# Optimization experiments

Hardware: AMD Instinct MI355X
Metric: run time of the kernel (lower is better)

## Reference

```python
import jax, jax.numpy as jnp
import numpy as np

B, N = 4, 512
H, NH, L = 64, 4, 3
HD = H // NH          # 16
NODE_F, EDGE_F = 18, 7
H4 = H // 4           # 16
FF = 4 * H            # 256


def _ln(x, g, b, eps=1e-5):
    m = jnp.mean(x, axis=-1, keepdims=True)
    v = jnp.mean((x - m) ** 2, axis=-1, keepdims=True)
    return (x - m) * jax.lax.rsqrt(v + eps) * g + b


def _leaky(x):
    return jnp.where(x >= 0, x, 0.2 * x)


def _spd(edge_mask):
    # Vectorized Floyd-Warshall, mirrors GraphTransformer._compute_spd_matrix
    n = edge_mask.shape[1]
    spd = jnp.where(edge_mask, 1.0, float(n)).astype(jnp.float32)
    i = jnp.arange(n)
    spd = spd.at[:, i, i].set(0.0)
    def body(k, s):
        col = jax.lax.dynamic_slice_in_dim(s, k, 1, axis=2)  # [B,N,1]
        row = jax.lax.dynamic_slice_in_dim(s, k, 1, axis=1)  # [B,1,N]
        return jnp.minimum(s, col + row)
    return jax.lax.fori_loop(0, n, body, spd)


def setup_inputs() -> dict:
    key = jax.random.key(0)
    ks = iter(jax.random.split(key, 64))
    def nrm(shape, s):
        return jax.random.normal(next(ks), shape, jnp.float32) * s
    inp = {}
    inp["node_features"] = jax.random.normal(next(ks), (B, N, NODE_F), jnp.float32)
    inp["edge_features"] = jax.random.normal(next(ks), (B, N, N, EDGE_F), jnp.float32)
    nm = jax.random.uniform(next(ks), (B, N)) < 0.9
    inp["node_mask"] = nm.at[:, 0].set(True)
    inp["edge_mask"] = jax.random.uniform(next(ks), (B, N, N)) < 0.05
    s_h = 1.0 / np.sqrt(H)
    inp["node_proj_w"] = nrm((NODE_F, H), 0.2)
    inp["node_proj_b"] = jnp.zeros((H,), jnp.float32)
    inp["edge_proj_w"] = nrm((EDGE_F, H), 0.2)
    inp["edge_proj_b"] = jnp.zeros((H,), jnp.float32)
    inp["wq"] = nrm((L, H, H), s_h)
    inp["wk"] = nrm((L, H, H), s_h)
    inp["wv"] = nrm((L, H, H), s_h)
    inp["eb1_w"] = nrm((L, H, H4), s_h)
    inp["eb1_b"] = jnp.zeros((L, H4), jnp.float32)
    inp["eb_ln_g"] = jnp.ones((L, H4), jnp.float32)
    inp["eb_ln_b"] = jnp.zeros((L, H4), jnp.float32)
    inp["eb2_w"] = nrm((L, H4, NH), 0.2)
    inp["eb2_b"] = jnp.zeros((L, NH), jnp.float32)
    inp["spd1_w"] = nrm((L, 1, H4), 0.5)
    inp["spd1_b"] = jnp.zeros((L, H4), jnp.float32)
    inp["spd2_w"] = nrm((L, H4, NH), 0.2)
    inp["spd2_b"] = jnp.zeros((L, NH), jnp.float32)
    inp["wo_w"] = nrm((L, H, H), s_h)
    inp["wo_b"] = jnp.zeros((L, H), jnp.float32)
    inp["ln1_g"] = jnp.ones((L, H), jnp.float32)
    inp["ln1_b"] = jnp.zeros((L, H), jnp.float32)
    inp["ln2_g"] = jnp.ones((L, H), jnp.float32)
    inp["ln2_b"] = jnp.zeros((L, H), jnp.float32)
    inp["ffn1_w"] = nrm((L, H, FF), s_h)
    inp["ffn1_b"] = jnp.zeros((L, FF), jnp.float32)
    inp["ffn2_w"] = nrm((L, FF, H), 1.0 / np.sqrt(FF))
    inp["ffn2_b"] = jnp.zeros((L, H), jnp.float32)
    inp["score1_w"] = nrm((2 * H, H), 1.0 / np.sqrt(2 * H))
    inp["score1_b"] = jnp.zeros((H,), jnp.float32)
    inp["score_ln_g"] = jnp.ones((H,), jnp.float32)
    inp["score_ln_b"] = jnp.zeros((H,), jnp.float32)
    inp["score2_w"] = nrm((H, 1), 0.1)
    inp["score2_b"] = jnp.zeros((1,), jnp.float32)
    return inp


def reference(node_features, edge_features, node_mask, edge_mask,
              node_proj_w, node_proj_b, edge_proj_w, edge_proj_b,
              wq, wk, wv,
              eb1_w, eb1_b, eb_ln_g, eb_ln_b, eb2_w, eb2_b,
              spd1_w, spd1_b, spd2_w, spd2_b,
              wo_w, wo_b, ln1_g, ln1_b, ln2_g, ln2_b,
              ffn1_w, ffn1_b, ffn2_w, ffn2_b,
              score1_w, score1_b, score_ln_g, score_ln_b, score2_w, score2_b):
    NEG = -1000000000.0
    h = node_features @ node_proj_w + node_proj_b            # [B,N,H]
    e = edge_features @ edge_proj_w + edge_proj_b            # [B,N,N,H]
    spd = _spd(edge_mask)
    spd_n = (jnp.clip(spd, 0.0, 10.0) / 10.0)[..., None]      # [B,N,N,1]
    scale = 1.0 / np.sqrt(HD)
    for l in range(L):
        Q = (h @ wq[l]).reshape(B, N, NH, HD)
        K = (h @ wk[l]).reshape(B, N, NH, HD)
        V = (h @ wv[l]).reshape(B, N, NH, HD)
        scores = jnp.einsum('bihd,bjhd->bhij', Q, K) * scale  # [B,NH,N,N]
        x = _leaky(_ln(e @ eb1_w[l] + eb1_b[l], eb_ln_g[l], eb_ln_b[l]))
        edge_bias = jnp.transpose(x @ eb2_w[l] + eb2_b[l], (0, 3, 1, 2))
        sb = _leaky(spd_n @ spd1_w[l] + spd1_b[l]) @ spd2_w[l] + spd2_b[l]
        spd_bias = jnp.transpose(sb, (0, 3, 1, 2))
        bias = jnp.where(edge_mask[:, None, :, :], edge_bias, spd_bias)
        scores = jnp.where(node_mask[:, None, None, :], scores + bias, NEG)
        attn = jax.nn.softmax(scores, axis=-1)
        out = jnp.einsum('bhij,bjhd->bihd', attn, V).reshape(B, N, H)
        out = out @ wo_w[l] + wo_b[l]
        h = _ln(h + out, ln1_g[l], ln1_b[l])
        ff = jax.nn.gelu(h @ ffn1_w[l] + ffn1_b[l], approximate=False) @ ffn2_w[l] + ffn2_b[l]
        h = _ln(h + ff, ln2_g[l], ln2_b[l])
    h_ego = jnp.broadcast_to(h[:, :1, :], (B, N - 1, H))
    hc = jnp.concatenate([h_ego, h[:, 1:, :]], axis=-1)       # [B,N-1,2H]
    x = _leaky(_ln(hc @ score1_w + score1_b, score_ln_g, score_ln_b))
    logits = (x @ score2_w + score2_b)[..., 0]                # [B,N-1]
    cand_mask = node_mask[:, 1:]
    no_cand = ~jnp.any(cand_mask, axis=-1)
    cand_mask = cand_mask.at[:, 0].set(cand_mask[:, 0] | no_cand)
    logits = jnp.where(cand_mask, logits, NEG)
    probs = jax.nn.softmax(logits, axis=-1)
    return probs, h
```

## Files before the change

### kernel.cpp

```cpp
#include <hip/hip_runtime.h>
#include <math.h>

typedef unsigned long long u64;
typedef unsigned int u32;

__device__ __forceinline__ float wsum(float x) {
#pragma unroll
    for (int o = 1; o < 64; o <<= 1) x += __shfl_xor(x, o);
    return x;
}
__device__ __forceinline__ float wmaxr(float x) {
#pragma unroll
    for (int o = 1; o < 64; o <<= 1) x = fmaxf(x, __shfl_xor(x, o));
    return x;
}

__global__ __launch_bounds__(256) void kA(
    const int* __restrict__ em, const float* __restrict__ nf,
    const float* __restrict__ npw, const float* __restrict__ npb,
    u64* __restrict__ adj, u32* __restrict__ elist, u32* __restrict__ rowCnt,
    float* __restrict__ hbuf)
{
    int t = threadIdx.x, wv = t >> 6, lane = t & 63;
    int g = blockIdx.x * 4 + wv;
    const int* emr = em + (size_t)g * 512;
    u32 run = 0;
#pragma unroll
    for (int s = 0; s < 8; ++s) {
        int j = s * 64 + lane;
        int v = emr[j];
        u64 bal = __ballot(v != 0);
        if (v != 0) {
            u32 slot = run + (u32)__popcll(bal & ((1ULL << lane) - 1ULL));
            if (slot < 96u) elist[g * 96 + slot] = (u32)j;
        }
        if (lane == 0) adj[(size_t)g * 8 + s] = bal;
        run += (u32)__popcll(bal);
    }
    if (lane == 0) rowCnt[g] = run < 96u ? run : 96u;
    float acc = npb[lane];
    const float* r = nf + (size_t)g * 18;
#pragma unroll
    for (int c = 0; c < 18; ++c) acc += r[c] * npw[c * 64 + lane];
    hbuf[(size_t)g * 64 + lane] = acc;
}

__global__ __launch_bounds__(256) void kB(
    const u64* __restrict__ adj, const float* __restrict__ ef,
    const u32* __restrict__ elist, const u32* __restrict__ rowCnt,
    const float* __restrict__ hbuf,
    const float* __restrict__ epw, const float* __restrict__ epb,
    const float* __restrict__ eb1w, const float* __restrict__ eb1b,
    const float* __restrict__ eblng, const float* __restrict__ eblnb,
    const float* __restrict__ eb2w, const float* __restrict__ eb2b,
    const float* __restrict__ wq, const float* __restrict__ wk, const float* __restrict__ wvw,
    unsigned char* __restrict__ spd, float* __restrict__ vals,
    float* __restrict__ Qb, float* __restrict__ KT, float* __restrict__ VT)
{
    __shared__ u64 adjL[4096];
    __shared__ u64 bfsS[4][24];
    __shared__ float MS[684];
    __shared__ u32 pool[384];
    __shared__ u32 offs[5];
    __shared__ u32 cA[4];
    __shared__ int votes[4];
    int t = threadIdx.x, wv = t >> 6, lane = t & 63;
    int g = blockIdx.x * 4 + wv;
    int b = g >> 9, srow = g & 511;
    {
        const float4* s = (const float4*)(adj + (size_t)b * 4096);
        float4* d = (float4*)adjL;
#pragma unroll
        for (int u = 0; u < 8; ++u) d[t + u * 256] = s[t + u * 256];
    }
    for (int u = t; u < 384; u += 256) {
        int l = u >> 7, r = u & 127, f = r >> 4, c = r & 15;
        const float* W1 = eb1w + l * 1024 + c;
        float s;
        if (f < 7) {
            s = 0.f;
            const float* ew = epw + f * 64;
            for (int k = 0; k < 64; ++k) s += ew[k] * W1[k * 16];
        } else {
            s = eb1b[l * 16 + c];
            for (int k = 0; k < 64; ++k) s += epb[k] * W1[k * 16];
        }
        MS[u] = s;
    }
    if (t < 192) MS[384 + t] = eb2w[t];
    if (t < 48) { MS[576 + t] = eblng[t]; MS[624 + t] = eblnb[t]; }
    if (t < 12) MS[672 + t] = eb2b[t];
    u64* vis = &bfsS[wv][0]; u64* fro = vis + 8; u64* nxt = vis + 16;
    if (lane < 8) {
        u64 iv = (lane == (srow >> 6)) ? (1ULL << (srow & 63)) : 0ULL;
        vis[lane] = iv; fro[lane] = iv; nxt[lane] = 0ULL;
    }
    __syncthreads();
    u64 myDist = 0x0A0A0A0A0A0A0A0AULL;
    if (lane == (srow >> 3)) myDist &= ~(0xFFULL << ((srow & 7) * 8));
    for (int d = 1; d <= 9; ++d) {
        int c = lane >> 3, w = lane & 7;
        u64 f = fro[c];
        u64 acc = 0ULL;
        while (f) {
            int k = (c << 6) + __builtin_ctzll(f);
            f &= f - 1;
            acc |= adjL[k * 8 + w];
        }
        if (acc) atomicOr(&nxt[w], acc);
        __syncthreads();
        u64 nw = 0ULL;
        if (lane < 8) {
            nw = nxt[lane] & ~vis[lane];
            vis[lane] |= nw; fro[lane] = nw; nxt[lane] = 0ULL;
        }
        u64 bal = __ballot(nw != 0ULL);
        if (lane == 0) votes[wv] = (bal != 0ULL) ? 1 : 0;
        __syncthreads();
        u64 fw = fro[lane >> 3];
        u32 bits = (u32)(fw >> ((lane & 7) * 8)) & 0xFFu;
        if (bits) {
            u64 bm = 0ULL;
#pragma unroll
            for (int kk = 0; kk < 8; ++kk) if (bits & (1u << kk)) bm |= 0xFFULL << (8 * kk);
            myDist = (myDist & ~bm) | ((0x0101010101010101ULL * (u64)(u32)d) & bm);
        }
        if (!(votes[0] | votes[1] | votes[2] | votes[3])) break;
    }
    ((u64*)spd)[(size_t)g * 64 + lane] = myDist;
    {
        float hv = hbuf[(size_t)g * 64 + lane];
        float aq = 0.f, ak = 0.f, av = 0.f;
        for (int k = 0; k < 64; ++k) {
            float hk = __shfl(hv, k);
            aq += hk * wq[k * 64 + lane];
            ak += hk * wk[k * 64 + lane];
            av += hk * wvw[k * 64 + lane];
        }
        Qb[(size_t)g * 64 + lane] = aq;
        KT[((size_t)(b * 64 + lane)) * 512 + srow] = ak;
        VT[((size_t)(b * 64 + lane)) * 512 + srow] = av;
    }
    u32 cnt = rowCnt[g];
    if (lane == 0) cA[wv] = cnt;
    __syncthreads();
    if (t == 0) {
        u32 a = 0;
        for (int i = 0; i < 4; ++i) { offs[i] = a; a += cA[i]; }
        offs[4] = a;
    }
    __syncthreads();
    u32 base = offs[wv];
    if (lane < (int)cnt)
        pool[base + lane] = ((u32)wv << 16) | ((u32)lane << 9) | elist[g * 96 + lane];
    if (lane + 64 < (int)cnt)
        pool[base + lane + 64] = ((u32)wv << 16) | ((u32)(lane + 64) << 9) | elist[g * 96 + lane + 64];
    __syncthreads();
    u32 tot = offs[4];
    for (u32 e = t; e < tot; e += 256) {
        u32 p = pool[e];
        int rl = (int)(p >> 16);
        u32 s = (p >> 9) & 127u;
        u32 j = p & 511u;
        int ge = blockIdx.x * 4 + rl;
        const float* e7 = ef + ((size_t)ge * 512 + j) * 7;
        float ff[7];
#pragma unroll
        for (int f = 0; f < 7; ++f) ff[f] = e7[f];
#pragma unroll 1
        for (int l = 0; l < 3; ++l) {
            float tt[16];
#pragma unroll
            for (int c = 0; c < 16; ++c) tt[c] = MS[(l * 8 + 7) * 16 + c];
#pragma unroll
            for (int f = 0; f < 7; ++f) {
                float fv = ff[f];
#pragma unroll
                for (int c = 0; c < 16; ++c) tt[c] += fv * MS[(l * 8 + f) * 16 + c];
            }
            float m = 0.f;
#pragma unroll
            for (int c = 0; c < 16; ++c) m += tt[c];
            m *= 0.0625f;
            float var = 0.f;
#pragma unroll
            for (int c = 0; c < 16; ++c) { float d = tt[c] - m; var += d * d; }
            var *= 0.0625f;
            float inv = rsqrtf(var + 1e-5f);
#pragma unroll
            for (int c = 0; c < 16; ++c) {
                float x = (tt[c] - m) * inv * MS[576 + l * 16 + c] + MS[624 + l * 16 + c];
                tt[c] = x >= 0.f ? x : 0.2f * x;
            }
#pragma unroll
            for (int hh = 0; hh < 4; ++hh) {
                float a = MS[672 + l * 4 + hh];
#pragma unroll
                for (int c = 0; c < 16; ++c) a += tt[c] * MS[384 + (l * 16 + c) * 4 + hh];
                vals[(u32)(l * 4 + hh) * 196608u + (u32)ge * 96u + s] = a;
            }
        }
    }
}

__global__ __launch_bounds__(256) void kAttn(
    const float* __restrict__ Qb, const float* __restrict__ KTin, const float* __restrict__ VTin,
    const unsigned char* __restrict__ spd, const u32* __restrict__ elist,
    const u32* __restrict__ rowCnt, const float* __restrict__ vals,
    const float* __restrict__ s1w, const float* __restrict__ s1b,
    const float* __restrict__ s2w, const float* __restrict__ s2b,
    const int* __restrict__ nm, int l, float* __restrict__ attO)
{
    __shared__ float kt[8192];
    __shared__ float bv[2048];
    int t = threadIdx.x, wv = t >> 6, lane = t & 63;
    int blk = blockIdx.x;
    int bh = blk >> 7, tile = blk & 127;
    int b = bh >> 2, hh = bh & 3;
    int rbase = tile * 4;
    int g = b * 512 + rbase + wv;
    {
        const float4* s = (const float4*)(KTin + ((size_t)(b * 64 + hh * 16)) * 512);
        float4* d = (float4*)kt;
#pragma unroll
        for (int u = 0; u < 8; ++u) d[t + u * 256] = s[t + u * 256];
    }
    float tval;
    {
        int li = lane < 11 ? lane : 10;
        float x = (float)li * 0.1f;
        float a = s2b[l * 4 + hh];
#pragma unroll
        for (int c = 0; c < 16; ++c) {
            float v = x * s1w[l * 16 + c] + s1b[l * 16 + c];
            v = v >= 0.f ? v : 0.2f * v;
            a += v * s2w[(l * 16 + c) * 4 + hh];
        }
        tval = a;
    }
    {
        const u32* sp = (const u32*)(spd + ((size_t)(b * 512 + rbase)) * 512);
#pragma unroll
        for (int p = 0; p < 2; ++p) {
            int i32 = t + p * 256;
            u32 w4 = sp[i32];
            float4 bb;
            bb.x = __shfl(tval, (int)(w4 & 255u));
            bb.y = __shfl(tval, (int)((w4 >> 8) & 255u));
            bb.z = __shfl(tval, (int)((w4 >> 16) & 255u));
            bb.w = __shfl(tval, (int)(w4 >> 24));
            ((float4*)bv)[i32] = bb;
        }
    }
    __syncthreads();
    u32 cnt = rowCnt[g];
    u32 vp = (u32)(l * 4 + hh) * 196608u;
    if (lane < (int)cnt) {
        u32 j = elist[g * 96 + lane];
        bv[wv * 512 + j] = vals[vp + (u32)g * 96u + lane];
    }
    if (lane + 64 < (int)cnt) {
        u32 j = elist[g * 96 + lane + 64];
        bv[wv * 512 + j] = vals[vp + (u32)g * 96u + lane + 64];
    }
    float madd[8];
#pragma unroll
    for (int c = 0; c < 8; ++c) madd[c] = (nm[b * 512 + c * 64 + lane] != 0) ? 0.f : -1e9f;
    float qrow = Qb[(size_t)g * 64 + lane];
    float q[16];
#pragma unroll
    for (int d = 0; d < 16; ++d) q[d] = __shfl(qrow, hh * 16 + d);
    float sc[8];
    float mx = -3e38f;
#pragma unroll
    for (int c = 0; c < 8; ++c) {
        int j = c * 64 + lane;
        float s = 0.f;
#pragma unroll
        for (int d = 0; d < 16; ++d) s += q[d] * kt[d * 512 + j];
        s = s * 0.25f + bv[wv * 512 + j] + madd[c];
        sc[c] = s;
        mx = fmaxf(mx, s);
    }
    mx = wmaxr(mx);
    float sm = 0.f;
#pragma unroll
    for (int c = 0; c < 8; ++c) { sc[c] = __expf(sc[c] - mx); sm += sc[c]; }
    float sminv = 1.0f / wsum(sm);
#pragma unroll
    for (int c = 0; c < 8; ++c) sc[c] *= sminv;
    __syncthreads();
    {
        const float4* s = (const float4*)(VTin + ((size_t)(b * 64 + hh * 16)) * 512);
        float4* d = (float4*)kt;
#pragma unroll
        for (int u = 0; u < 8; ++u) d[t + u * 256] = s[t + u * 256];
    }
    __syncthreads();
    float acc[16];
#pragma unroll
    for (int d = 0; d < 16; ++d) acc[d] = 0.f;
#pragma unroll
    for (int c = 0; c < 8; ++c) {
        int j = c * 64 + lane;
#pragma unroll
        for (int d = 0; d < 16; ++d) acc[d] += sc[c] * kt[d * 512 + j];
    }
#pragma unroll
    for (int d = 0; d < 16; ++d) {
        acc[d] += __shfl_xor(acc[d], 16);
        acc[d] += __shfl_xor(acc[d], 32);
    }
    float* scr = bv + wv * 272;
    if (lane < 16) {
#pragma unroll
        for (int d = 0; d < 16; ++d) scr[lane * 17 + d] = acc[d];
    }
    if (lane < 16) {
        float o = 0.f;
#pragma unroll
        for (int m = 0; m < 16; ++m) o += scr[m * 17 + lane];
        attO[(size_t)g * 64 + hh * 16 + lane] = o;
    }
}

__global__ __launch_bounds__(256) void kLF(
    const float* __restrict__ attO,
    const float* __restrict__ wow, const float* __restrict__ wob,
    const float* __restrict__ ln1g, const float* __restrict__ ln1b,
    const float* __restrict__ f1w, const float* __restrict__ f1b,
    const float* __restrict__ f2w, const float* __restrict__ f2b,
    const float* __restrict__ ln2g, const float* __restrict__ ln2b,
    const float* __restrict__ wqn, const float* __restrict__ wkn, const float* __restrict__ wvn,
    const float* __restrict__ sc1w, const float* __restrict__ sc1b,
    float* __restrict__ hbuf, float* __restrict__ QbOut,
    float* __restrict__ KTout, float* __restrict__ VTout,
    float* __restrict__ egoAcc, int l, float* __restrict__ out)
{
    int t = threadIdx.x, wv = t >> 6, lane = t & 63;
    int g = blockIdx.x * 4 + wv;
    int b = g >> 9, srow = g & 511;
    float hv = hbuf[(size_t)g * 64 + lane];
    float att = attO[(size_t)g * 64 + lane];
    float h1;
    {
        float a = wob[l * 64 + lane];
        const float* Wo = wow + l * 4096;
        for (int k = 0; k < 64; ++k) a += __shfl(att, k) * Wo[k * 64 + lane];
        float xx = a + hv;
        float mn = wsum(xx) * 0.015625f;
        float d = xx - mn;
        float var = wsum(d * d) * 0.015625f;
        h1 = d * rsqrtf(var + 1e-5f) * ln1g[l * 64 + lane] + ln1b[l * 64 + lane];
    }
    float hn;
    {
        const float* W1 = f1w + l * 16384;
        const float* W2 = f2w + l * 16384;
        float a1[4];
#pragma unroll
        for (int m = 0; m < 4; ++m) a1[m] = f1b[l * 256 + m * 64 + lane];
        for (int k = 0; k < 64; ++k) {
            float hk = __shfl(h1, k);
#pragma unroll
            for (int m = 0; m < 4; ++m) a1[m] += hk * W1[k * 256 + m * 64 + lane];
        }
        float ffv[4];
#pragma unroll
        for (int m = 0; m < 4; ++m) {
            float u = a1[m];
            ffv[m] = 0.5f * u * (1.0f + erff(u * 0.70710678118654752f));
        }
        float a2 = 0.f;
#pragma unroll 1
        for (int m = 0; m < 4; ++m) {
            for (int ll = 0; ll < 64; ++ll) {
                a2 += __shfl(ffv[m], ll) * W2[(m * 64 + ll) * 64 + lane];
            }
        }
        float xx = a2 + f2b[l * 64 + lane] + h1;
        float mn = wsum(xx) * 0.015625f;
        float d = xx - mn;
        float var = wsum(d * d) * 0.015625f;
        hn = d * rsqrtf(var + 1e-5f) * ln2g[l * 64 + lane] + ln2b[l * 64 + lane];
    }
    hbuf[(size_t)g * 64 + lane] = hn;
    if (l == 2) {
        out[2044 + (size_t)g * 64 + lane] = hn;
        if (srow == 0) {
            float ea = sc1b[lane];
            for (int k = 0; k < 64; ++k) ea += __shfl(hn, k) * sc1w[k * 64 + lane];
            egoAcc[b * 64 + lane] = ea;
        }
    } else {
        float aq = 0.f, ak = 0.f, av = 0.f;
        for (int k = 0; k < 64; ++k) {
            float hk = __shfl(hn, k);
            aq += hk * wqn[k * 64 + lane];
            ak += hk * wkn[k * 64 + lane];
            av += hk * wvn[k * 64 + lane];
        }
        QbOut[(size_t)g * 64 + lane] = aq;
        KTout[((size_t)(b * 64 + lane)) * 512 + srow] = ak;
        VTout[((size_t)(b * 64 + lane)) * 512 + srow] = av;
    }
}

__global__ __launch_bounds__(256) void kS(
    const float* __restrict__ hbuf, const float* __restrict__ egoAcc,
    const float* __restrict__ s1w,
    const float* __restrict__ lng, const float* __restrict__ lnb,
    const float* __restrict__ s2w, const float* __restrict__ s2b,
    float* __restrict__ logits)
{
    int t = threadIdx.x, wv = t >> 6, lane = t & 63;
    int wid = blockIdx.x * 4 + wv;
    if (wid >= 2044) return;
    int bb = wid / 511; int jj = wid % 511; int j = jj + 1;
    float cand = hbuf[((size_t)(bb * 512 + j)) * 64 + lane];
    float acc = egoAcc[bb * 64 + lane];
    for (int k = 0; k < 64; ++k) acc += __shfl(cand, k) * s1w[(64 + k) * 64 + lane];
    float mn = wsum(acc) * 0.015625f;
    float d = acc - mn;
    float var = wsum(d * d) * 0.015625f;
    float x = d * rsqrtf(var + 1e-5f) * lng[lane] + lnb[lane];
    x = x >= 0.f ? x : 0.2f * x;
    float p = wsum(x * s2w[lane]);
    if (lane == 0) logits[wid] = p + s2b[0];
}

__global__ __launch_bounds__(512) void kP(
    const float* __restrict__ logits, const int* __restrict__ nmask, float* __restrict__ out)
{
    __shared__ float red[512];
    __shared__ int anyf;
    int b = blockIdx.x; int t = threadIdx.x;
    bool cand = false;
    if (t < 511) cand = nmask[b * 512 + 1 + t] != 0;
    if (t == 0) anyf = 0;
    __syncthreads();
    if (cand) atomicOr(&anyf, 1);
    __syncthreads();
    if (t == 0 && anyf == 0) cand = true;
    float val = -3e38f;
    if (t < 511) val = cand ? logits[b * 511 + t] : -1e9f;
    red[t] = val; __syncthreads();
    for (int s = 256; s > 0; s >>= 1) { if (t < s) red[t] = fmaxf(red[t], red[t + s]); __syncthreads(); }
    float m = red[0]; __syncthreads();
    float p = (t < 511) ? __expf(val - m) : 0.f;
    red[t] = p; __syncthreads();
    for (int s = 256; s > 0; s >>= 1) { if (t < s) red[t] += red[t + s]; __syncthreads(); }
    float inv = 1.0f / red[0];
    if (t < 511) out[b * 511 + t] = p * inv;
}

extern "C" void kernel_launch(void* const* d_in, const int* in_sizes, int n_in,
                              void* d_out, int out_size, void* d_ws, size_t ws_size,
                              hipStream_t stream) {
    const float* nf    = (const float*)d_in[0];
    const float* ef    = (const float*)d_in[1];
    const int*   nm    = (const int*)d_in[2];
    const int*   em    = (const int*)d_in[3];
    const float* npw   = (const float*)d_in[4];
    const float* npb   = (const float*)d_in[5];
    const float* epw   = (const float*)d_in[6];
    const float* epb   = (const float*)d_in[7];
    const float* wq    = (const float*)d_in[8];
    const float* wk    = (const float*)d_in[9];
    const float* wv    = (const float*)d_in[10];
    const float* eb1w  = (const float*)d_in[11];
    const float* eb1b  = (const float*)d_in[12];
    const float* eblng = (const float*)d_in[13];
    const float* eblnb = (const float*)d_in[14];
    const float* eb2w  = (const float*)d_in[15];
    const float* eb2b  = (const float*)d_in[16];
    const float* s1wv  = (const float*)d_in[17];
    const float* s1bv  = (const float*)d_in[18];
    const float* s2wv  = (const float*)d_in[19];
    const float* s2bv  = (const float*)d_in[20];
    const float* wow   = (const float*)d_in[21];
    const float* wob   = (const float*)d_in[22];
    const float* ln1g  = (const float*)d_in[23];
    const float* ln1b  = (const float*)d_in[24];
    const float* ln2g  = (const float*)d_in[25];
    const float* ln2b  = (const float*)d_in[26];
    const float* f1w   = (const float*)d_in[27];
    const float* f1b   = (const float*)d_in[28];
    const float* f2w   = (const float*)d_in[29];
    const float* f2b   = (const float*)d_in[30];
    const float* sc1w  = (const float*)d_in[31];
    const float* sc1b  = (const float*)d_in[32];
    const float* sclng = (const float*)d_in[33];
    const float* sclnb = (const float*)d_in[34];
    const float* sc2w  = (const float*)d_in[35];
    const float* sc2b  = (const float*)d_in[36];

    char* W = (char*)d_ws;
    u64*   adj    = (u64*)(W + 0);
    unsigned char* spd = (unsigned char*)(W + 131072);
    u32*   elist  = (u32*)(W + 1179648);
    u32*   rowCnt = (u32*)(W + 1966080);
    float* vals   = (float*)(W + 1974272);
    float* hbuf   = (float*)(W + 11411456);
    float* Qb     = (float*)(W + 11935744);
    float* KT0    = (float*)(W + 12460032);
    float* VT0    = (float*)(W + 12984320);
    float* KT1    = (float*)(W + 13508608);
    float* VT1    = (float*)(W + 14032896);
    float* logits = (float*)(W + 14557184);
    float* egoAcc = (float*)(W + 14565376);
    float* attO   = (float*)(W + 14566400);

    float* out = (float*)d_out;

    kA<<<512, 256, 0, stream>>>(em, nf, npw, npb, adj, elist, rowCnt, hbuf);
    kB<<<512, 256, 0, stream>>>(adj, ef, elist, rowCnt, hbuf, epw, epb,
                                eb1w, eb1b, eblng, eblnb, eb2w, eb2b,
                                wq, wk, wv, spd, vals, Qb, KT0, VT0);

    kAttn<<<2048, 256, 0, stream>>>(Qb, KT0, VT0, spd, elist, rowCnt, vals,
                                    s1wv, s1bv, s2wv, s2bv, nm, 0, attO);
    kLF<<<512, 256, 0, stream>>>(attO, wow, wob, ln1g, ln1b, f1w, f1b, f2w, f2b,
                                 ln2g, ln2b, wq + 4096, wk + 4096, wv + 4096,
                                 sc1w, sc1b, hbuf, Qb, KT1, VT1, egoAcc, 0, out);

    kAttn<<<2048, 256, 0, stream>>>(Qb, KT1, VT1, spd, elist, rowCnt, vals,
                                    s1wv, s1bv, s2wv, s2bv, nm, 1, attO);
    kLF<<<512, 256, 0, stream>>>(attO, wow, wob, ln1g, ln1b, f1w, f1b, f2w, f2b,
                                 ln2g, ln2b, wq + 8192, wk + 8192, wv + 8192,
                                 sc1w, sc1b, hbuf, Qb, KT0, VT0, egoAcc, 1, out);

    kAttn<<<2048, 256, 0, stream>>>(Qb, KT0, VT0, spd, elist, rowCnt, vals,
                                    s1wv, s1bv, s2wv, s2bv, nm, 2, attO);
    kLF<<<512, 256, 0, stream>>>(attO, wow, wob, ln1g, ln1b, f1w, f1b, f2w, f2b,
                                 ln2g, ln2b, wq, wk, wv,
                                 sc1w, sc1b, hbuf, Qb, KT1, VT1, egoAcc, 2, out);

    kS<<<511, 256, 0, stream>>>(hbuf, egoAcc, s1wv ? sc1w : sc1w, sclng, sclnb, sc2w, sc2b, logits);
    kP<<<4, 512, 0, stream>>>(logits, nm, out);
}
```

Baseline: 315.8 us.

## Fuse per-layer attention into FFN kernel and merge scoring with softmax

Each layer's attention is folded into the layer/FFN kernel. Every block now loops serially over the four heads for its own four rows and keeps the attention output in shared memory, so the attO global round trip and one launch per layer go away. The candidate-scoring and final softmax kernels are merged into a single 4-block, 1024-thread kernel, with logits held in shared memory. In exchange, the attention grid shrinks from 2048 blocks to 512 and head processing is serialized, and the scoring stage runs on only four blocks. Both changes reduce parallelism.

```diff
diff --git a/kernel.cpp b/kernel.cpp
--- a/kernel.cpp
+++ b/kernel.cpp
@@ -203,129 +203,13 @@
     }
 }
 
-__global__ __launch_bounds__(256) void kAttn(
+__global__ __launch_bounds__(256, 2) void kL(
     const float* __restrict__ Qb, const float* __restrict__ KTin, const float* __restrict__ VTin,
     const unsigned char* __restrict__ spd, const u32* __restrict__ elist,
     const u32* __restrict__ rowCnt, const float* __restrict__ vals,
     const float* __restrict__ s1w, const float* __restrict__ s1b,
     const float* __restrict__ s2w, const float* __restrict__ s2b,
-    const int* __restrict__ nm, int l, float* __restrict__ attO)
-{
-    __shared__ float kt[8192];
-    __shared__ float bv[2048];
-    int t = threadIdx.x, wv = t >> 6, lane = t & 63;
-    int blk = blockIdx.x;
-    int bh = blk >> 7, tile = blk & 127;
-    int b = bh >> 2, hh = bh & 3;
-    int rbase = tile * 4;
-    int g = b * 512 + rbase + wv;
-    {
-        const float4* s = (const float4*)(KTin + ((size_t)(b * 64 + hh * 16)) * 512);
-        float4* d = (float4*)kt;
-#pragma unroll
-        for (int u = 0; u < 8; ++u) d[t + u * 256] = s[t + u * 256];
-    }
-    float tval;
-    {
-        int li = lane < 11 ? lane : 10;
-        float x = (float)li * 0.1f;
-        float a = s2b[l * 4 + hh];
-#pragma unroll
-        for (int c = 0; c < 16; ++c) {
-            float v = x * s1w[l * 16 + c] + s1b[l * 16 + c];
-            v = v >= 0.f ? v : 0.2f * v;
-            a += v * s2w[(l * 16 + c) * 4 + hh];
-        }
-        tval = a;
-    }
-    {
-        const u32* sp = (const u32*)(spd + ((size_t)(b * 512 + rbase)) * 512);
-#pragma unroll
-        for (int p = 0; p < 2; ++p) {
-            int i32 = t + p * 256;
-            u32 w4 = sp[i32];
-            float4 bb;
-            bb.x = __shfl(tval, (int)(w4 & 255u));
-            bb.y = __shfl(tval, (int)((w4 >> 8) & 255u));
-            bb.z = __shfl(tval, (int)((w4 >> 16) & 255u));
-            bb.w = __shfl(tval, (int)(w4 >> 24));
-            ((float4*)bv)[i32] = bb;
-        }
-    }
-    __syncthreads();
-    u32 cnt = rowCnt[g];
-    u32 vp = (u32)(l * 4 + hh) * 196608u;
-    if (lane < (int)cnt) {
-        u32 j = elist[g * 96 + lane];
-        bv[wv * 512 + j] = vals[vp + (u32)g * 96u + lane];
-    }
-    if (lane + 64 < (int)cnt) {
-        u32 j = elist[g * 96 + lane + 64];
-        bv[wv * 512 + j] = vals[vp + (u32)g * 96u + lane + 64];
-    }
-    float madd[8];
-#pragma unroll
-    for (int c = 0; c < 8; ++c) madd[c] = (nm[b * 512 + c * 64 + lane] != 0) ? 0.f : -1e9f;
-    float qrow = Qb[(size_t)g * 64 + lane];
-    float q[16];
-#pragma unroll
-    for (int d = 0; d < 16; ++d) q[d] = __shfl(qrow, hh * 16 + d);
-    float sc[8];
-    float mx = -3e38f;
-#pragma unroll
-    for (int c = 0; c < 8; ++c) {
-        int j = c * 64 + lane;
-        float s = 0.f;
-#pragma unroll
-        for (int d = 0; d < 16; ++d) s += q[d] * kt[d * 512 + j];
-        s = s * 0.25f + bv[wv * 512 + j] + madd[c];
-        sc[c] = s;
-        mx = fmaxf(mx, s);
-    }
-    mx = wmaxr(mx);
-    float sm = 0.f;
-#pragma unroll
-    for (int c = 0; c < 8; ++c) { sc[c] = __expf(sc[c] - mx); sm += sc[c]; }
-    float sminv = 1.0f / wsum(sm);
-#pragma unroll
-    for (int c = 0; c < 8; ++c) sc[c] *= sminv;
-    __syncthreads();
-    {
-        const float4* s = (const float4*)(VTin + ((size_t)(b * 64 + hh * 16)) * 512);
-        float4* d = (float4*)kt;
-#pragma unroll
-        for (int u = 0; u < 8; ++u) d[t + u * 256] = s[t + u * 256];
-    }
-    __syncthreads();
-    float acc[16];
-#pragma unroll
-    for (int d = 0; d < 16; ++d) acc[d] = 0.f;
-#pragma unroll
-    for (int c = 0; c < 8; ++c) {
-        int j = c * 64 + lane;
-#pragma unroll
-        for (int d = 0; d < 16; ++d) acc[d] += sc[c] * kt[d * 512 + j];
-    }
-#pragma unroll
-    for (int d = 0; d < 16; ++d) {
-        acc[d] += __shfl_xor(acc[d], 16);
-        acc[d] += __shfl_xor(acc[d], 32);
-    }
-    float* scr = bv + wv * 272;
-    if (lane < 16) {
-#pragma unroll
-        for (int d = 0; d < 16; ++d) scr[lane * 17 + d] = acc[d];
-    }
-    if (lane < 16) {
-        float o = 0.f;
-#pragma unroll
-        for (int m = 0; m < 16; ++m) o += scr[m * 17 + lane];
-        attO[(size_t)g * 64 + hh * 16 + lane] = o;
-    }
-}
-
-__global__ __launch_bounds__(256) void kLF(
-    const float* __restrict__ attO,
+    const int* __restrict__ nm,
     const float* __restrict__ wow, const float* __restrict__ wob,
     const float* __restrict__ ln1g, const float* __restrict__ ln1b,
     const float* __restrict__ f1w, const float* __restrict__ f1b,
@@ -337,16 +221,116 @@
     float* __restrict__ KTout, float* __restrict__ VTout,
     float* __restrict__ egoAcc, int l, float* __restrict__ out)
 {
+    __shared__ float kt[8192];
+    __shared__ float bv[2048];
+    __shared__ float ATTO[256];
     int t = threadIdx.x, wv = t >> 6, lane = t & 63;
-    int g = blockIdx.x * 4 + wv;
+    int blk = blockIdx.x;
+    int g = blk * 4 + wv;
     int b = g >> 9, srow = g & 511;
     float hv = hbuf[(size_t)g * 64 + lane];
-    float att = attO[(size_t)g * 64 + lane];
+    float qrow = Qb[(size_t)g * 64 + lane];
+    const unsigned char* sprow = spd + (size_t)g * 512;
+    unsigned char sb[8];
+#pragma unroll
+    for (int c = 0; c < 8; ++c) sb[c] = sprow[c * 64 + lane];
+    float madd[8];
+#pragma unroll
+    for (int c = 0; c < 8; ++c) madd[c] = (nm[b * 512 + c * 64 + lane] != 0) ? 0.f : -1e9f;
+    u32 cnt = rowCnt[g];
+    u32 ej0 = 0, ej1 = 0;
+    if (lane < (int)cnt) ej0 = elist[g * 96 + lane] & 511u;
+    if (lane + 64 < (int)cnt) ej1 = elist[g * 96 + lane + 64] & 511u;
+
+#pragma unroll 1
+    for (int hh = 0; hh < 4; ++hh) {
+        __syncthreads();
+        {
+            const float4* s = (const float4*)(KTin + ((size_t)(b * 64 + hh * 16)) * 512);
+            float4* d = (float4*)kt;
+#pragma unroll
+            for (int u = 0; u < 8; ++u) d[t + u * 256] = s[t + u * 256];
+        }
+        float tval;
+        {
+            int li = lane < 11 ? lane : 10;
+            float x = (float)li * 0.1f;
+            float a = s2b[l * 4 + hh];
+#pragma unroll
+            for (int c = 0; c < 16; ++c) {
+                float v = x * s1w[l * 16 + c] + s1b[l * 16 + c];
+                v = v >= 0.f ? v : 0.2f * v;
+                a += v * s2w[(l * 16 + c) * 4 + hh];
+            }
+            tval = a;
+        }
+#pragma unroll
+        for (int c = 0; c < 8; ++c) bv[wv * 512 + c * 64 + lane] = __shfl(tval, (int)sb[c]);
+        u32 vp = (u32)(l * 4 + hh) * 196608u;
+        if (lane < (int)cnt) bv[wv * 512 + ej0] = vals[vp + (u32)g * 96u + lane];
+        if (lane + 64 < (int)cnt) bv[wv * 512 + ej1] = vals[vp + (u32)g * 96u + lane + 64];
+        __syncthreads();
+        float q[16];
+#pragma unroll
+        for (int d = 0; d < 16; ++d) q[d] = __shfl(qrow, hh * 16 + d);
+        float sc[8];
+        float mx = -3e38f;
+#pragma unroll
+        for (int c = 0; c < 8; ++c) {
+            int j = c * 64 + lane;
+            float s = 0.f;
+#pragma unroll
+            for (int d = 0; d < 16; ++d) s += q[d] * kt[d * 512 + j];
+            s = s * 0.25f + bv[wv * 512 + j] + madd[c];
+            sc[c] = s;
+            mx = fmaxf(mx, s);
+        }
+        mx = wmaxr(mx);
+        float sm = 0.f;
+#pragma unroll
+        for (int c = 0; c < 8; ++c) { sc[c] = __expf(sc[c] - mx); sm += sc[c]; }
+        float sminv = 1.0f / wsum(sm);
+#pragma unroll
+        for (int c = 0; c < 8; ++c) sc[c] *= sminv;
+        __syncthreads();
+        {
+            const float4* s = (const float4*)(VTin + ((size_t)(b * 64 + hh * 16)) * 512);
+            float4* d = (float4*)kt;
+#pragma unroll
+            for (int u = 0; u < 8; ++u) d[t + u * 256] = s[t + u * 256];
+        }
+        __syncthreads();
+        float acc[16];
+#pragma unroll
+        for (int d = 0; d < 16; ++d) acc[d] = 0.f;
+#pragma unroll
+        for (int c = 0; c < 8; ++c) {
+            int j = c * 64 + lane;
+#pragma unroll
+            for (int d = 0; d < 16; ++d) acc[d] += sc[c] * kt[d * 512 + j];
+        }
+#pragma unroll
+        for (int d = 0; d < 16; ++d) {
+            acc[d] += __shfl_xor(acc[d], 16);
+            acc[d] += __shfl_xor(acc[d], 32);
+        }
+        float* scr = bv + wv * 272;
+        if (lane < 16) {
+#pragma unroll
+            for (int d = 0; d < 16; ++d) scr[lane * 17 + d] = acc[d];
+        }
+        if (lane < 16) {
+            float o = 0.f;
+#pragma unroll
+            for (int m = 0; m < 16; ++m) o += scr[m * 17 + lane];
+            ATTO[wv * 64 + hh * 16 + lane] = o;
+        }
+    }
     float h1;
     {
         float a = wob[l * 64 + lane];
         const float* Wo = wow + l * 4096;
-        for (int k = 0; k < 64; ++k) a += __shfl(att, k) * Wo[k * 64 + lane];
+        for (int k = 0; k < 64; ++k) a += ATTO[wv * 64 + k] * Wo[k * 64 + lane];
         float xx = a + hv;
         float mn = wsum(xx) * 0.015625f;
         float d = xx - mn;
@@ -406,50 +390,60 @@
     }
 }
 
-__global__ __launch_bounds__(256) void kS(
+__global__ __launch_bounds__(1024) void kSP(
     const float* __restrict__ hbuf, const float* __restrict__ egoAcc,
     const float* __restrict__ s1w,
     const float* __restrict__ lng, const float* __restrict__ lnb,
     const float* __restrict__ s2w, const float* __restrict__ s2b,
-    float* __restrict__ logits)
+    const int* __restrict__ nm, float* __restrict__ out)
 {
-    int t = threadIdx.x, wv = t >> 6, lane = t & 63;
-    int wid = blockIdx.x * 4 + wv;
-    if (wid >= 2044) return;
-    int bb = wid / 511; int jj = wid % 511; int j = jj + 1;
-    float cand = hbuf[((size_t)(bb * 512 + j)) * 64 + lane];
-    float acc = egoAcc[bb * 64 + lane];
-    for (int k = 0; k < 64; ++k) acc += __shfl(cand, k) * s1w[(64 + k) * 64 + lane];
-    float mn = wsum(acc) * 0.015625f;
-    float d = acc - mn;
-    float var = wsum(d * d) * 0.015625f;
-    float x = d * rsqrtf(var + 1e-5f) * lng[lane] + lnb[lane];
-    x = x >= 0.f ? x : 0.2f * x;
-    float p = wsum(x * s2w[lane]);
-    if (lane == 0) logits[wid] = p + s2b[0];
-}
-
-__global__ __launch_bounds__(512) void kP(
-    const float* __restrict__ logits, const int* __restrict__ nmask, float* __restrict__ out)
-{
+    __shared__ float lgt[512];
     __shared__ float red[512];
     __shared__ int anyf;
-    int b = blockIdx.x; int t = threadIdx.x;
+    int b = blockIdx.x, t = threadIdx.x;
+    int wave = t >> 6, lane = t & 63;
+    if (t == 0) anyf = 0;
+    float eacc = egoAcc[b * 64 + lane];
+    float s2wl = s2w[lane];
+    float lngl = lng[lane], lnbl = lnb[lane];
+    float s2b0 = s2b[0];
+#pragma unroll 1
+    for (int jj = wave; jj < 511; jj += 16) {
+        int j = jj + 1;
+        float cand = hbuf[((size_t)(b * 512 + j)) * 64 + lane];
+        float acc = eacc;
+        for (int k = 0; k < 64; ++k) acc += __shfl(cand, k) * s1w[(64 + k) * 64 + lane];
+        float mn = wsum(acc) * 0.015625f;
+        float d = acc - mn;
+        float var = wsum(d * d) * 0.015625f;
+        float x = d * rsqrtf(var + 1e-5f) * lngl + lnbl;
+        x = x >= 0.f ? x : 0.2f * x;
+        float p = wsum(x * s2wl);
+        if (lane == 0) lgt[jj] = p + s2b0;
+    }
+    __syncthreads();
     bool cand = false;
-    if (t < 511) cand = nmask[b * 512 + 1 + t] != 0;
-    if (t == 0) anyf = 0;
-    __syncthreads();
+    if (t < 511) cand = nm[b * 512 + 1 + t] != 0;
     if (cand) atomicOr(&anyf, 1);
     __syncthreads();
     if (t == 0 && anyf == 0) cand = true;
     float val = -3e38f;
-    if (t < 511) val = cand ? logits[b * 511 + t] : -1e9f;
-    red[t] = val; __syncthreads();
-    for (int s = 256; s > 0; s >>= 1) { if (t < s) red[t] = fmaxf(red[t], red[t + s]); __syncthreads(); }
-    float m = red[0]; __syncthreads();
+    if (t < 511) val = cand ? lgt[t] : -1e9f;
+    if (t < 512) red[t] = val;
+    __syncthreads();
+    for (int s = 256; s > 0; s >>= 1) {
+        if (t < s) red[t] = fmaxf(red[t], red[t + s]);
+        __syncthreads();
+    }
+    float m = red[0];
+    __syncthreads();
     float p = (t < 511) ? __expf(val - m) : 0.f;
-    red[t] = p; __syncthreads();
-    for (int s = 256; s > 0; s >>= 1) { if (t < s) red[t] += red[t + s]; __syncthreads(); }
+    if (t < 512) red[t] = p;
+    __syncthreads();
+    for (int s = 256; s > 0; s >>= 1) {
+        if (t < s) red[t] += red[t + s];
+        __syncthreads();
+    }
     float inv = 1.0f / red[0];
     if (t < 511) out[b * 511 + t] = p * inv;
 }
@@ -507,9 +501,7 @@
     float* VT0    = (float*)(W + 12984320);
     float* KT1    = (float*)(W + 13508608);
     float* VT1    = (float*)(W + 14032896);
-    float* logits = (float*)(W + 14557184);
-    float* egoAcc = (float*)(W + 14565376);
-    float* attO   = (float*)(W + 14566400);
+    float* egoAcc = (float*)(W + 14557184);
 
     float* out = (float*)d_out;
 
@@ -518,24 +510,21 @@
                                 eb1w, eb1b, eblng, eblnb, eb2w, eb2b,
                                 wq, wk, wv, spd, vals, Qb, KT0, VT0);
 
-    kAttn<<<2048, 256, 0, stream>>>(Qb, KT0, VT0, spd, elist, rowCnt, vals,
-                                    s1wv, s1bv, s2wv, s2bv, nm, 0, attO);
-    kLF<<<512, 256, 0, stream>>>(attO, wow, wob, ln1g, ln1b, f1w, f1b, f2w, f2b,
-                                 ln2g, ln2b, wq + 4096, wk + 4096, wv + 4096,
-                                 sc1w, sc1b, hbuf, Qb, KT1, VT1, egoAcc, 0, out);
-
-    kAttn<<<2048, 256, 0, stream>>>(Qb, KT1, VT1, spd, elist, rowCnt, vals,
-                                    s1wv, s1bv, s2wv, s2bv, nm, 1, attO);
-    kLF<<<512, 256, 0, stream>>>(attO, wow, wob, ln1g, ln1b, f1w, f1b, f2w, f2b,
-                                 ln2g, ln2b, wq + 8192, wk + 8192, wv + 8192,
-                                 sc1w, sc1b, hbuf, Qb, KT0, VT0, egoAcc, 1, out);
-
-    kAttn<<<2048, 256, 0, stream>>>(Qb, KT0, VT0, spd, elist, rowCnt, vals,
-                                    s1wv, s1bv, s2wv, s2bv, nm, 2, attO);
-    kLF<<<512, 256, 0, stream>>>(attO, wow, wob, ln1g, ln1b, f1w, f1b, f2w, f2b,
-                                 ln2g, ln2b, wq, wk, wv,
-                                 sc1w, sc1b, hbuf, Qb, KT1, VT1, egoAcc, 2, out);
-
-    kS<<<511, 256, 0, stream>>>(hbuf, egoAcc, s1wv ? sc1w : sc1w, sclng, sclnb, sc2w, sc2b, logits);
-    kP<<<4, 512, 0, stream>>>(logits, nm, out);
-}
+    kL<<<512, 256, 0, stream>>>(Qb, KT0, VT0, spd, elist, rowCnt, vals,
+                                s1wv, s1bv, s2wv, s2bv, nm,
+                                wow, wob, ln1g, ln1b, f1w, f1b, f2w, f2b, ln2g, ln2b,
+                                wq + 4096, wk + 4096, wv + 4096, sc1w, sc1b,
+                                hbuf, Qb, KT1, VT1, egoAcc, 0, out);
+    kL<<<512, 256, 0, stream>>>(Qb, KT1, VT1, spd, elist, rowCnt, vals,
+                                s1wv, s1bv, s2wv, s2bv, nm,
+                                wow, wob, ln1g, ln1b, f1w, f1b, f2w, f2b, ln2g, ln2b,
+                                wq + 8192, wk + 8192, wv + 8192, sc1w, sc1b,
+                                hbuf, Qb, KT0, VT0, egoAcc, 1, out);
+    kL<<<512, 256, 0, stream>>>(Qb, KT0, VT0, spd, elist, rowCnt, vals,
+                                s1wv, s1bv, s2wv, s2bv, nm,
+                                wow, wob, ln1g, ln1b, f1w, f1b, f2w, f2b, ln2g, ln2b,
+                                wq, wk, wv, sc1w, sc1b,
+                                hbuf, Qb, KT1, VT1, egoAcc, 2, out);
+
+    kSP<<<4, 1024, 0, stream>>>(hbuf, egoAcc, sc1w, sclng, sclnb, sc2w, sc2b, nm, out);
+}
```

Result: slower. 427.7 us (+35.5%).

## Process four query rows per wavefront in attention to reuse K/V tiles

Applied to the files above, without the earlier changes.

The attention kernel now assigns 16 rows per block (4 rows per wavefront) instead of 4. Each K and V column read from shared memory is reused across four queries, and each K/V staging load is amortised over four times as many rows. The grid shrinks from 2048 to 512 blocks and launch_bounds requests 2 blocks per SM. The cost is much higher register use (q[4][16], sc[8][4], acc[4][16]), a larger bias buffer in shared memory (64 KB total per block), and fewer blocks to spread across the GPU, which risks lower occupancy.

```diff
diff --git a/kernel.cpp b/kernel.cpp
--- a/kernel.cpp
+++ b/kernel.cpp
@@ -203,7 +203,7 @@
     }
 }
 
-__global__ __launch_bounds__(256) void kAttn(
+__global__ __launch_bounds__(256, 2) void kAttn(
     const float* __restrict__ Qb, const float* __restrict__ KTin, const float* __restrict__ VTin,
     const unsigned char* __restrict__ spd, const u32* __restrict__ elist,
     const u32* __restrict__ rowCnt, const float* __restrict__ vals,
@@ -212,13 +212,19 @@
     const int* __restrict__ nm, int l, float* __restrict__ attO)
 {
     __shared__ float kt[8192];
-    __shared__ float bv[2048];
+    __shared__ float bv[8192];
     int t = threadIdx.x, wv = t >> 6, lane = t & 63;
-    int blk = blockIdx.x;
-    int bh = blk >> 7, tile = blk & 127;
+    int bh = blockIdx.x >> 5;
+    int tile = blockIdx.x & 31;
     int b = bh >> 2, hh = bh & 3;
-    int rbase = tile * 4;
-    int g = b * 512 + rbase + wv;
+    int i0 = tile * 16;
+    int rbase = i0 + wv * 4;
+    float qv = Qb[((size_t)(b * 512 + rbase + (lane >> 4))) * 64 + hh * 16 + (lane & 15)];
+    float q[4][16];
+#pragma unroll
+    for (int r = 0; r < 4; ++r)
+#pragma unroll
+        for (int d = 0; d < 16; ++d) q[r][d] = __shfl(qv, r * 16 + d);
     {
         const float4* s = (const float4*)(KTin + ((size_t)(b * 64 + hh * 16)) * 512);
         float4* d = (float4*)kt;
@@ -239,9 +245,9 @@
         tval = a;
     }
     {
-        const u32* sp = (const u32*)(spd + ((size_t)(b * 512 + rbase)) * 512);
-#pragma unroll
-        for (int p = 0; p < 2; ++p) {
+        const u32* sp = (const u32*)(spd + ((size_t)(b * 512 + i0)) * 512);
+#pragma unroll
+        for (int p = 0; p < 8; ++p) {
             int i32 = t + p * 256;
             u32 w4 = sp[i32];
             float4 bb;
@@ -253,42 +259,49 @@
         }
     }
     __syncthreads();
-    u32 cnt = rowCnt[g];
     u32 vp = (u32)(l * 4 + hh) * 196608u;
-    if (lane < (int)cnt) {
-        u32 j = elist[g * 96 + lane];
-        bv[wv * 512 + j] = vals[vp + (u32)g * 96u + lane];
-    }
-    if (lane + 64 < (int)cnt) {
-        u32 j = elist[g * 96 + lane + 64];
-        bv[wv * 512 + j] = vals[vp + (u32)g * 96u + lane + 64];
-    }
-    float madd[8];
-#pragma unroll
-    for (int c = 0; c < 8; ++c) madd[c] = (nm[b * 512 + c * 64 + lane] != 0) ? 0.f : -1e9f;
-    float qrow = Qb[(size_t)g * 64 + lane];
-    float q[16];
-#pragma unroll
-    for (int d = 0; d < 16; ++d) q[d] = __shfl(qrow, hh * 16 + d);
-    float sc[8];
-    float mx = -3e38f;
+#pragma unroll
+    for (int rr = 0; rr < 4; ++rr) {
+        int g = b * 512 + rbase + rr;
+        u32 cnt = rowCnt[g];
+        for (u32 s = lane; s < cnt; s += 64u) {
+            u32 j = elist[g * 96 + s] & 511u;
+            bv[(wv * 4 + rr) * 512 + j] = vals[vp + (u32)g * 96u + s];
+        }
+    }
+    const int* nmb = nm + b * 512;
+    float sc[8][4];
+    float mx[4] = {-3e38f, -3e38f, -3e38f, -3e38f};
 #pragma unroll
     for (int c = 0; c < 8; ++c) {
         int j = c * 64 + lane;
-        float s = 0.f;
-#pragma unroll
-        for (int d = 0; d < 16; ++d) s += q[d] * kt[d * 512 + j];
-        s = s * 0.25f + bv[wv * 512 + j] + madd[c];
-        sc[c] = s;
-        mx = fmaxf(mx, s);
-    }
-    mx = wmaxr(mx);
-    float sm = 0.f;
-#pragma unroll
-    for (int c = 0; c < 8; ++c) { sc[c] = __expf(sc[c] - mx); sm += sc[c]; }
-    float sminv = 1.0f / wsum(sm);
-#pragma unroll
-    for (int c = 0; c < 8; ++c) sc[c] *= sminv;
+        float ktv[16];
+#pragma unroll
+        for (int d = 0; d < 16; ++d) ktv[d] = kt[d * 512 + j];
+        float madd = (nmb[j] != 0) ? 0.f : -1e9f;
+#pragma unroll
+        for (int r = 0; r < 4; ++r) {
+            float s = 0.f;
+#pragma unroll
+            for (int d = 0; d < 16; ++d) s += q[r][d] * ktv[d];
+            s = s * 0.25f + bv[(wv * 4 + r) * 512 + j] + madd;
+            sc[c][r] = s;
+            mx[r] = fmaxf(mx[r], s);
+        }
+    }
+#pragma unroll
+    for (int r = 0; r < 4; ++r) mx[r] = wmaxr(mx[r]);
+    float sm[4] = {0.f, 0.f, 0.f, 0.f};
+#pragma unroll
+    for (int c = 0; c < 8; ++c)
+#pragma unroll
+        for (int r = 0; r < 4; ++r) { sc[c][r] = __expf(sc[c][r] - mx[r]); sm[r] += sc[c][r]; }
+#pragma unroll
+    for (int r = 0; r < 4; ++r) sm[r] = 1.0f / wsum(sm[r]);
+#pragma unroll
+    for (int c = 0; c < 8; ++c)
+#pragma unroll
+        for (int r = 0; r < 4; ++r) sc[c][r] *= sm[r];
     __syncthreads();
     {
         const float4* s = (const float4*)(VTin + ((size_t)(b * 64 + hh * 16)) * 512);
@@ -297,31 +310,39 @@
         for (int u = 0; u < 8; ++u) d[t + u * 256] = s[t + u * 256];
     }
     __syncthreads();
-    float acc[16];
-#pragma unroll
-    for (int d = 0; d < 16; ++d) acc[d] = 0.f;
+    float acc[4][16];
+#pragma unroll
+    for (int r = 0; r < 4; ++r)
+#pragma unroll
+        for (int d = 0; d < 16; ++d) acc[r][d] = 0.f;
 #pragma unroll
     for (int c = 0; c < 8; ++c) {
         int j = c * 64 + lane;
 #pragma unroll
-        for (int d = 0; d < 16; ++d) acc[d] += sc[c] * kt[d * 512 + j];
-    }
-#pragma unroll
-    for (int d = 0; d < 16; ++d) {
-        acc[d] += __shfl_xor(acc[d], 16);
-        acc[d] += __shfl_xor(acc[d], 32);
-    }
-    float* scr = bv + wv * 272;
+        for (int d = 0; d < 16; ++d) {
+            float v = kt[d * 512 + j];
+#pragma unroll
+            for (int r = 0; r < 4; ++r) acc[r][d] += sc[c][r] * v;
+        }
+    }
+#pragma unroll
+    for (int r = 0; r < 4; ++r)
+#pragma unroll
+        for (int d = 0; d < 16; ++d) {
+            acc[r][d] += __shfl_xor(acc[r][d], 16);
+            acc[r][d] += __shfl_xor(acc[r][d], 32);
+        }
+    float* scr = bv + wv * 2048;
     if (lane < 16) {
 #pragma unroll
-        for (int d = 0; d < 16; ++d) scr[lane * 17 + d] = acc[d];
-    }
-    if (lane < 16) {
-        float o = 0.f;
-#pragma unroll
-        for (int m = 0; m < 16; ++m) o += scr[m * 17 + lane];
-        attO[(size_t)g * 64 + hh * 16 + lane] = o;
-    }
+        for (int r = 0; r < 4; ++r)
+#pragma unroll
+            for (int d = 0; d < 16; ++d) scr[lane * 65 + r * 16 + d] = acc[r][d];
+    }
+    float o = 0.f;
+#pragma unroll
+    for (int m = 0; m < 16; ++m) o += scr[m * 65 + lane];
+    attO[((size_t)(b * 512 + rbase + (lane >> 4))) * 64 + hh * 16 + (lane & 15)] = o;
 }
 
 __global__ __launch_bounds__(256) void kLF(
@@ -518,24 +539,24 @@
                                 eb1w, eb1b, eblng, eblnb, eb2w, eb2b,
                                 wq, wk, wv, spd, vals, Qb, KT0, VT0);
 
-    kAttn<<<2048, 256, 0, stream>>>(Qb, KT0, VT0, spd, elist, rowCnt, vals,
-                                    s1wv, s1bv, s2wv, s2bv, nm, 0, attO);
+    kAttn<<<512, 256, 0, stream>>>(Qb, KT0, VT0, spd, elist, rowCnt, vals,
+                                   s1wv, s1bv, s2wv, s2bv, nm, 0, attO);
     kLF<<<512, 256, 0, stream>>>(attO, wow, wob, ln1g, ln1b, f1w, f1b, f2w, f2b,
                                  ln2g, ln2b, wq + 4096, wk + 4096, wv + 4096,
                                  sc1w, sc1b, hbuf, Qb, KT1, VT1, egoAcc, 0, out);
 
-    kAttn<<<2048, 256, 0, stream>>>(Qb, KT1, VT1, spd, elist, rowCnt, vals,
-                                    s1wv, s1bv, s2wv, s2bv, nm, 1, attO);
+    kAttn<<<512, 256, 0, stream>>>(Qb, KT1, VT1, spd, elist, rowCnt, vals,
+                                   s1wv, s1bv, s2wv, s2bv, nm, 1, attO);
     kLF<<<512, 256, 0, stream>>>(attO, wow, wob, ln1g, ln1b, f1w, f1b, f2w, f2b,
                                  ln2g, ln2b, wq + 8192, wk + 8192, wv + 8192,
                                  sc1w, sc1b, hbuf, Qb, KT0, VT0, egoAcc, 1, out);
 
-    kAttn<<<2048, 256, 0, stream>>>(Qb, KT0, VT0, spd, elist, rowCnt, vals,
-                                    s1wv, s1bv, s2wv, s2bv, nm, 2, attO);
+    kAttn<<<512, 256, 0, stream>>>(Qb, KT0, VT0, spd, elist, rowCnt, vals,
+                                   s1wv, s1bv, s2wv, s2bv, nm, 2, attO);
     kLF<<<512, 256, 0, stream>>>(attO, wow, wob, ln1g, ln1b, f1w, f1b, f2w, f2b,
                                  ln2g, ln2b, wq, wk, wv,
                                  sc1w, sc1b, hbuf, Qb, KT1, VT1, egoAcc, 2, out);
 
-    kS<<<511, 256, 0, stream>>>(hbuf, egoAcc, s1wv ? sc1w : sc1w, sclng, sclnb, sc2w, sc2b, logits);
+    kS<<<511, 256, 0, stream>>>(hbuf, egoAcc, sc1w, sclng, sclnb, sc2w, sc2b, logits);
     kP<<<4, 512, 0, stream>>>(logits, nm, out);
 }
```

New measurement: 299.4 us. -5.2%, faster.
